# Performance work log

Hardware: AMD Instinct MI355X
Metric: run time of the kernel (lower is better)

Reference implementation:

```python
import jax, jax.numpy as jnp
import numpy as np

B, M, D, H, C = 256, 512, 768, 8, 768


def setup_inputs() -> dict:
    key = jax.random.key(0)
    ks = jax.random.split(key, 12)
    rn = lambda k, shp, s=1.0: jax.random.normal(k, shp, dtype=jnp.float32) * s
    w = 1.0 / np.sqrt(D)
    return dict(
        controller_state=rn(ks[0], (B, C)),
        write_data=rn(ks[1], (B, D)),
        memory=rn(ks[2], (M, D), 0.1),
        in_proj_w=rn(ks[3], (3 * D, D), w), in_proj_b=jnp.zeros((3 * D,), jnp.float32),
        out_w=rn(ks[4], (D, D), w), out_b=jnp.zeros((D,), jnp.float32),
        read_w=rn(ks[5], (D, C), w), read_b=jnp.zeros((D,), jnp.float32),
        write_w=rn(ks[6], (D, C), w), write_b=jnp.zeros((D,), jnp.float32),
        erase_w=rn(ks[7], (D, C), w), erase_b=jnp.zeros((D,), jnp.float32),
        ug_w=rn(ks[8], (1, C + D), w), ug_b=jnp.zeros((1,), jnp.float32),
        fg_w=rn(ks[9], (1, C + D), w), fg_b=jnp.zeros((1,), jnp.float32),
    )


def _mha(q, kv, in_proj_w, in_proj_b, out_w, out_b, num_heads):
    # q: [B,1,D] query, kv: [B,M,D] keys=values. Matches torch.nn.MultiheadAttention
    # (batch_first, eval mode -> no dropout, average_attn_weights=True).
    b, m, d = kv.shape
    dh = d // num_heads
    wq, wk, wv = jnp.split(in_proj_w, 3, axis=0)
    bq, bk, bv = jnp.split(in_proj_b, 3, axis=0)
    qh = (q @ wq.T + bq).reshape(b, 1, num_heads, dh).transpose(0, 2, 1, 3)   # [B,H,1,dh]
    kh = (kv @ wk.T + bk).reshape(b, m, num_heads, dh).transpose(0, 2, 1, 3)  # [B,H,M,dh]
    vh = (kv @ wv.T + bv).reshape(b, m, num_heads, dh).transpose(0, 2, 1, 3)
    scores = jnp.einsum('bhqd,bhkd->bhqk', qh, kh) / jnp.sqrt(jnp.float32(dh))
    attn = jax.nn.softmax(scores, axis=-1)                                    # [B,H,1,M]
    ctx = jnp.einsum('bhqk,bhkd->bhqd', attn, vh)
    ctx = ctx.transpose(0, 2, 1, 3).reshape(b, 1, d)
    out = ctx @ out_w.T + out_b
    return out, attn.mean(axis=1)  # out [B,1,D], weights averaged over heads [B,1,M]


def reference(controller_state, write_data, memory, in_proj_w, in_proj_b,
              out_w, out_b, read_w, read_b, write_w, write_b,
              erase_w, erase_b, ug_w, ug_b, fg_w, fg_b):
    b = controller_state.shape[0]
    memory_batch = jnp.broadcast_to(memory[None], (b,) + memory.shape)        # [B,M,D]

    read_key = (controller_state @ read_w.T + read_b)[:, None, :]             # [B,1,D]
    read_data, _ = _mha(read_key, memory_batch, in_proj_w, in_proj_b, out_w, out_b, H)
    read_data = read_data[:, 0, :]                                            # [B,D]

    write_key = (controller_state @ write_w.T + write_b)[:, None, :]
    erase_vec = jax.nn.sigmoid(controller_state @ erase_w.T + erase_b)[:, None, :]  # [B,1,D]
    _, write_weights = _mha(write_key, memory_batch, in_proj_w, in_proj_b, out_w, out_b, H)
    ww = write_weights[:, 0, :]                                               # [B,M]

    combined = jnp.concatenate([controller_state, read_data], axis=-1)        # [B,C+D]
    ug = jax.nn.sigmoid(combined @ ug_w.T + ug_b)                             # [B,1]
    fg = jax.nn.sigmoid(combined @ fg_w.T + fg_b)                             # [B,1]

    erase_term = ww[:, :, None] * erase_vec * fg[:, :, None]                  # [B,M,D]
    write_term = ww[:, :, None] * write_data[:, None, :] * ug[:, :, None]     # [B,M,D]
    updated_memory = memory_batch + (write_term - erase_term)
    return read_data, updated_memory
```

## Files before the change

kernel.cpp:

```cpp
#include <hip/hip_runtime.h>
#include <hip/hip_bf16.h>
#include <math.h>

#define B_ 256
#define M_ 512
#define D_ 768
#define H_ 8
#define DH_ 96
#define C_ 768

typedef float  f32x4_t __attribute__((ext_vector_type(4)));
typedef short  s16x8   __attribute__((ext_vector_type(8)));
typedef unsigned short u16;

__device__ __forceinline__ u16 cvt_bf16(float f) {
    __hip_bfloat16 h = __float2bfloat16(f);
    union { __hip_bfloat16 h; u16 u; } v; v.h = h;
    return v.u;
}
__device__ __forceinline__ float bf16_f32(u16 h) {
    union { unsigned int u; float f; } v; v.u = ((unsigned int)h) << 16;
    return v.f;
}

#define ACC_INIT {{0,0,0,0},{0,0,0,0},{0,0,0,0},{0,0,0,0}}
#define SCALE_ 0.10206207261596577f

template<int BK>
__device__ __forceinline__ void mm64b(
    const u16* __restrict__ A, int lda, const u16* __restrict__ B, int ldb,
    int ksteps, int bRowClamp, u16* lA, u16* lB, f32x4_t* acc, int nfrag)
{
    constexpr int NL = BK / 32;
    const int t = threadIdx.x;
    const int srow = t >> 2, kq = t & 3;
    const int l = t & 63, w = t >> 6;
    const int brow = srow < bRowClamp ? srow : bRowClamp;

    s16x8 va[NL], vb[NL];
    #pragma unroll
    for (int c = 0; c < NL; ++c) {
        const int ko = (kq * NL + c) * 8;
        va[c] = *reinterpret_cast<const s16x8*>(A + (size_t)srow * lda + ko);
        vb[c] = *reinterpret_cast<const s16x8*>(B + (size_t)brow * ldb + ko);
    }

    for (int ks = 0; ks < ksteps; ++ks) {
        __syncthreads();
        #pragma unroll
        for (int c = 0; c < NL; ++c) {
            const int kb = kq * NL + c;
            *reinterpret_cast<s16x8*>(lA + (kb * 64 + srow) * 8) = va[c];
            *reinterpret_cast<s16x8*>(lB + (kb * 64 + srow) * 8) = vb[c];
        }
        __syncthreads();
        if (ks + 1 < ksteps) {
            #pragma unroll
            for (int c = 0; c < NL; ++c) {
                const int ko = (ks + 1) * BK + (kq * NL + c) * 8;
                va[c] = *reinterpret_cast<const s16x8*>(A + (size_t)srow * lda + ko);
                vb[c] = *reinterpret_cast<const s16x8*>(B + (size_t)brow * ldb + ko);
            }
        }
        #pragma unroll
        for (int ksub = 0; ksub < NL; ++ksub) {
            const int kb = (l >> 4) + ksub * 4;
            s16x8 af = *reinterpret_cast<const s16x8*>(lA + (kb * 64 + w * 16 + (l & 15)) * 8);
            #pragma unroll
            for (int nb = 0; nb < 4; ++nb) {
                if (nb < nfrag) {
                    s16x8 bf = *reinterpret_cast<const s16x8*>(lB + (kb * 64 + nb * 16 + (l & 15)) * 8);
                    acc[nb] = __builtin_amdgcn_mfma_f32_16x16x32_bf16(af, bf, acc[nb], 0, 0, 0);
                }
            }
        }
    }
}

__device__ __forceinline__ void epilogue_f32(
    const f32x4_t* acc, float* out, int ldo, int m0, int n0,
    const float* bias, int act, int nfrag)
{
    const int t = threadIdx.x, l = t & 63, w = t >> 6;
    const int mbase = m0 + w * 16 + (l >> 4) * 4;
    #pragma unroll
    for (int nb = 0; nb < 4; ++nb) {
        if (nb >= nfrag) break;
        const int col = n0 + nb * 16 + (l & 15);
        const float bv = bias ? bias[col] : 0.0f;
        #pragma unroll
        for (int r = 0; r < 4; ++r) {
            float v = acc[nb][r] + bv;
            if (act) v = 1.0f / (1.0f + expf(-v));
            out[(size_t)(mbase + r) * ldo + col] = v;
        }
    }
}

__device__ __forceinline__ void epilogue_bf16(
    const f32x4_t* acc, u16* out, int ldo, int m0, int n0,
    const float* bias, int nfrag)
{
    const int t = threadIdx.x, l = t & 63, w = t >> 6;
    const int mbase = m0 + w * 16 + (l >> 4) * 4;
    #pragma unroll
    for (int nb = 0; nb < 4; ++nb) {
        if (nb >= nfrag) break;
        const int col = n0 + nb * 16 + (l & 15);
        const float bv = bias ? bias[col] : 0.0f;
        #pragma unroll
        for (int r = 0; r < 4; ++r)
            out[(size_t)(mbase + r) * ldo + col] = cvt_bf16(acc[nb][r] + bv);
    }
}

__global__ __launch_bounds__(256) void conv_kernel(
    const float* __restrict__ mem, const float* __restrict__ cs,
    const float* __restrict__ ipw, const float* __restrict__ rw,
    const float* __restrict__ www, const float* __restrict__ ew,
    const float* __restrict__ outw, const float* __restrict__ outb,
    const float* __restrict__ ugw, const float* __restrict__ ugb,
    const float* __restrict__ fgw, const float* __restrict__ fgb,
    u16* __restrict__ memb, u16* __restrict__ csb, u16* __restrict__ ipwb,
    u16* __restrict__ rwb, u16* __restrict__ wwwb, u16* __restrict__ ewb,
    u16* __restrict__ outwb, float* __restrict__ vg, float* __restrict__ gc)
{
    __shared__ float sred[256];
    const int bid = blockIdx.x, t = threadIdx.x;

    if (bid < 2304) {
        const float* src; u16* dst; int base;
        if      (bid < 192)  { src = mem;  dst = memb;  base = bid; }
        else if (bid < 288)  { src = cs;   dst = csb;   base = bid - 192; }
        else if (bid < 1152) { src = ipw;  dst = ipwb;  base = bid - 288; }
        else if (bid < 1440) { src = rw;   dst = rwb;   base = bid - 1152; }
        else if (bid < 1728) { src = www;  dst = wwwb;  base = bid - 1440; }
        else if (bid < 2016) { src = ew;   dst = ewb;   base = bid - 1728; }
        else                 { src = outw; dst = outwb; base = bid - 2016; }
        const size_t i = ((size_t)base * 256 + t) * 8;
        float4 x = *reinterpret_cast<const float4*>(src + i);
        float4 y = *reinterpret_cast<const float4*>(src + i + 4);
        s16x8 o;
        o[0]=cvt_bf16(x.x); o[1]=cvt_bf16(x.y); o[2]=cvt_bf16(x.z); o[3]=cvt_bf16(x.w);
        o[4]=cvt_bf16(y.x); o[5]=cvt_bf16(y.y); o[6]=cvt_bf16(y.z); o[7]=cvt_bf16(y.w);
        *reinterpret_cast<s16x8*>(dst + i) = o;
    } else {
        const int lid = bid - 2304;
        const int v = lid / 12, kt = lid % 12;
        const float* gw = v == 0 ? ugw : fgw;
        const int c = t & 63, g = t >> 6;
        const int col = kt * 64 + c;
        float acc = 0.f;
        #pragma unroll 4
        for (int i = 0; i < 192; ++i) {
            const int row = g * 192 + i;
            acc += outw[(size_t)row * 768 + col] * gw[768 + row];
        }
        sred[t] = acc;
        __syncthreads();
        if (g == 0)
            vg[v * 768 + col] = sred[c] + sred[64 + c] + sred[128 + c] + sred[192 + c];
        if (kt == 0) {
            __syncthreads();
            float cp = outb[t] * gw[768 + t] + outb[t + 256] * gw[768 + t + 256]
                     + outb[t + 512] * gw[768 + t + 512];
            sred[t] = cp; __syncthreads();
            #pragma unroll
            for (int off = 128; off > 0; off >>= 1) {
                if (t < off) sred[t] += sred[t + off];
                __syncthreads();
            }
            if (t == 0) gc[v] = sred[0] + (v == 0 ? ugb[0] : fgb[0]);
        }
    }
}

__global__ __launch_bounds__(256) void stage1_kernel(
    const u16* __restrict__ memb, const u16* __restrict__ csb,
    const u16* __restrict__ ipwb, const float* __restrict__ ipb,
    const u16* __restrict__ rwb, const float* __restrict__ rb,
    const u16* __restrict__ wwwb, const float* __restrict__ ww_b,
    const u16* __restrict__ ewb, const float* __restrict__ eb,
    u16* __restrict__ khb, u16* __restrict__ vhT,
    u16* __restrict__ rwkeysb, float* __restrict__ erase)
{
    __shared__ u16 lA[8192], lB[8192];
    f32x4_t acc[4] = ACC_INIT;
    const int bid = blockIdx.x;
    if (bid < 192) {
        const int mt = bid / 24, nt = bid % 24;
        mm64b<64>(memb + (size_t)mt * 64 * 768, 768,
                  ipwb + (size_t)768 * 768 + (size_t)nt * 64 * 768, 768,
                  12, 63, lA, lB, acc, 4);
        const int t = threadIdx.x, l = t & 63, w = t >> 6;
        const int mbase = mt * 64 + w * 16 + (l >> 4) * 4;
        if (nt < 12) {
            #pragma unroll
            for (int nb = 0; nb < 4; ++nb) {
                const int col = nt * 64 + nb * 16 + (l & 15);
                const float bv = ipb[768 + col];
                #pragma unroll
                for (int r = 0; r < 4; ++r)
                    khb[(size_t)(mbase + r) * 768 + col] = cvt_bf16(acc[nb][r] + bv);
            }
        } else {
            #pragma unroll
            for (int nb = 0; nb < 4; ++nb) {
                const int cg = (nt - 12) * 64 + nb * 16 + (l & 15);
                const int h = cg / 96, d = cg % 96;
                const float bv = ipb[1536 + cg];
                u16* dst = vhT + ((size_t)h * 96 + d) * 512;
                #pragma unroll
                for (int r = 0; r < 4; ++r)
                    dst[mbase + r] = cvt_bf16(acc[nb][r] + bv);
            }
        }
    } else if (bid < 240) {
        const int lid = bid - 192, mt = lid / 12, nt = lid % 12;
        mm64b<64>(csb + (size_t)mt * 64 * 768, 768, rwb + (size_t)nt * 64 * 768, 768,
                  12, 63, lA, lB, acc, 4);
        epilogue_bf16(acc, rwkeysb, 768, mt * 64, nt * 64, rb, 4);
    } else if (bid < 288) {
        const int lid = bid - 240, mt = lid / 12, nt = lid % 12;
        mm64b<64>(csb + (size_t)mt * 64 * 768, 768, wwwb + (size_t)nt * 64 * 768, 768,
                  12, 63, lA, lB, acc, 4);
        epilogue_bf16(acc, rwkeysb + (size_t)256 * 768, 768, mt * 64, nt * 64, ww_b, 4);
    } else {
        const int lid = bid - 288, mt = lid / 12, nt = lid % 12;
        mm64b<64>(csb + (size_t)mt * 64 * 768, 768, ewb + (size_t)nt * 64 * 768, 768,
                  12, 63, lA, lB, acc, 4);
        epilogue_f32(acc, erase, 768, mt * 64, nt * 64, eb, 1, 4);
    }
}

__global__ __launch_bounds__(256) void stage2_kernel(
    const u16* __restrict__ rwkeysb, const u16* __restrict__ ipwb,
    const float* __restrict__ ipb, u16* __restrict__ qrwb)
{
    __shared__ u16 lA[8192], lB[8192];
    f32x4_t acc[4] = ACC_INIT;
    const int mt = blockIdx.x / 12, nt = blockIdx.x % 12;
    mm64b<64>(rwkeysb + (size_t)mt * 64 * 768, 768, ipwb + (size_t)nt * 64 * 768, 768,
              12, 63, lA, lB, acc, 4);
    epilogue_bf16(acc, qrwb, 768, mt * 64, nt * 64, ipb, 4);
}

__global__ __launch_bounds__(256) void scores_kernel(
    const u16* __restrict__ qrwb, const u16* __restrict__ khb, u16* __restrict__ E)
{
    __shared__ u16 lA[2048], lB[2048];
    f32x4_t acc[4] = ACC_INIT;
    const int h = blockIdx.y;
    const int mt = blockIdx.x >> 3, nt = blockIdx.x & 7;
    mm64b<32>(qrwb + (size_t)mt * 64 * 768 + h * 96, 768,
              khb + (size_t)nt * 64 * 768 + h * 96, 768, 3, 63, lA, lB, acc, 4);
    const int t = threadIdx.x, l = t & 63, w = t >> 6;
    const int mbase = mt * 64 + w * 16 + (l >> 4) * 4;
    #pragma unroll
    for (int nb = 0; nb < 4; ++nb) {
        const int col = nt * 64 + nb * 16 + (l & 15);
        #pragma unroll
        for (int r = 0; r < 4; ++r) {
            const float e = expf(fminf(acc[nb][r] * SCALE_, 30.0f));
            E[((size_t)h * 512 + mbase + r) * 512 + col] = cvt_bf16(e);
        }
    }
}

__global__ __launch_bounds__(256) void pv_kernel(
    const u16* __restrict__ E, const u16* __restrict__ vhT, u16* __restrict__ ctxb)
{
    __shared__ u16 lA[8192], lB[8192];
    __shared__ float rinv[64];
    f32x4_t acc[4] = ACC_INIT;
    const int h = blockIdx.z, mt = blockIdx.x, nt = blockIdx.y;
    const int n0 = nt * 64;
    const int nfrag = nt == 0 ? 4 : 2;
    const int bclamp = nt == 0 ? 63 : 31;

    const u16* A  = E + ((size_t)h * 512 + mt * 64) * 512;
    const u16* Bv = vhT + ((size_t)h * 96 + n0) * 512;

    const int t = threadIdx.x;
    const int srow = t >> 2, kq = t & 3;
    const int l = t & 63, w = t >> 6;
    const int brow = srow < bclamp ? srow : bclamp;

    s16x8 va[2], vb[2];
    #pragma unroll
    for (int c = 0; c < 2; ++c) {
        const int ko = (kq * 2 + c) * 8;
        va[c] = *reinterpret_cast<const s16x8*>(A + (size_t)srow * 512 + ko);
        vb[c] = *reinterpret_cast<const s16x8*>(Bv + (size_t)brow * 512 + ko);
    }

    float rs = 0.f;
    for (int ks = 0; ks < 8; ++ks) {
        __syncthreads();
        #pragma unroll
        for (int c = 0; c < 2; ++c) {
            const int kb = kq * 2 + c;
            *reinterpret_cast<s16x8*>(lA + (kb * 64 + srow) * 8) = va[c];
            *reinterpret_cast<s16x8*>(lB + (kb * 64 + srow) * 8) = vb[c];
        }
        #pragma unroll
        for (int c = 0; c < 2; ++c)
            #pragma unroll
            for (int j = 0; j < 8; ++j)
                rs += bf16_f32((u16)va[c][j]);
        __syncthreads();
        if (ks + 1 < 8) {
            #pragma unroll
            for (int c = 0; c < 2; ++c) {
                const int ko = (ks + 1) * 64 + (kq * 2 + c) * 8;
                va[c] = *reinterpret_cast<const s16x8*>(A + (size_t)srow * 512 + ko);
                vb[c] = *reinterpret_cast<const s16x8*>(Bv + (size_t)brow * 512 + ko);
            }
        }
        #pragma unroll
        for (int ksub = 0; ksub < 2; ++ksub) {
            const int kb = (l >> 4) + ksub * 4;
            s16x8 af = *reinterpret_cast<const s16x8*>(lA + (kb * 64 + w * 16 + (l & 15)) * 8);
            #pragma unroll
            for (int nb = 0; nb < 4; ++nb) {
                if (nb < nfrag) {
                    s16x8 bf = *reinterpret_cast<const s16x8*>(lB + (kb * 64 + nb * 16 + (l & 15)) * 8);
                    acc[nb] = __builtin_amdgcn_mfma_f32_16x16x32_bf16(af, bf, acc[nb], 0, 0, 0);
                }
            }
        }
    }
    rs += __shfl_xor(rs, 1);
    rs += __shfl_xor(rs, 2);
    if (kq == 0) rinv[srow] = 1.0f / rs;
    __syncthreads();

    const int mbase = w * 16 + (l >> 4) * 4;
    #pragma unroll
    for (int nb = 0; nb < 4; ++nb) {
        if (nb >= nfrag) break;
        const int col = n0 + nb * 16 + (l & 15);
        #pragma unroll
        for (int r = 0; r < 4; ++r) {
            const float v = acc[nb][r] * rinv[mbase + r];
            ctxb[(size_t)(mt * 64 + mbase + r) * 768 + h * 96 + col] = cvt_bf16(v);
        }
    }
}

__global__ __launch_bounds__(256) void gatesww_kernel(
    const u16* __restrict__ ctxb,
    const float* __restrict__ cs, const float* __restrict__ wdta,
    const float* __restrict__ erase,
    const float* __restrict__ ugw, const float* __restrict__ fgw,
    const float* __restrict__ vg, const float* __restrict__ gc,
    const u16* __restrict__ E,
    float* __restrict__ delta, float* __restrict__ wwb)
{
    const int bid = blockIdx.x, t = threadIdx.x;
    if (bid < 256) {
        const int b = bid;
        __shared__ float red[8];
        float pu = 0.f, pf = 0.f;
        #pragma unroll
        for (int c = 0; c < 3; ++c) {
            const int i = t + c * 256;
            const float cv = cs[(size_t)b * 768 + i];
            const float xv = bf16_f32(ctxb[(size_t)b * 768 + i]);
            pu += cv * ugw[i] + xv * vg[i];
            pf += cv * fgw[i] + xv * vg[768 + i];
        }
        const int w = t >> 6, l = t & 63;
        #pragma unroll
        for (int off = 32; off > 0; off >>= 1) {
            pu += __shfl_xor(pu, off);
            pf += __shfl_xor(pf, off);
        }
        if (l == 0) { red[w] = pu; red[4 + w] = pf; }
        __syncthreads();
        const float ug = 1.0f / (1.0f + expf(-(red[0] + red[1] + red[2] + red[3] + gc[0])));
        const float fg = 1.0f / (1.0f + expf(-(red[4] + red[5] + red[6] + red[7] + gc[1])));
        #pragma unroll
        for (int c = 0; c < 3; ++c) {
            const int i = t + c * 256;
            delta[(size_t)b * 768 + i] = wdta[(size_t)b * 768 + i] * ug
                                       - erase[(size_t)b * 768 + i] * fg;
        }
    } else {
        const int b = bid - 256;
        __shared__ float linv8[8];
        const int w = t >> 6, l = t & 63;
        #pragma unroll
        for (int hh = 0; hh < 2; ++hh) {
            const int h = w * 2 + hh;
            const u16* row = E + ((size_t)h * 512 + 256 + b) * 512;
            float s = 0.f;
            #pragma unroll
            for (int c = 0; c < 8; ++c) s += bf16_f32(row[c * 64 + l]);
            #pragma unroll
            for (int off = 32; off > 0; off >>= 1) s += __shfl_xor(s, off);
            if (l == 0) linv8[h] = 1.0f / s;
        }
        __syncthreads();
        #pragma unroll
        for (int mm_ = 0; mm_ < 2; ++mm_) {
            const int m = t + mm_ * 256;
            float s = 0.f;
            #pragma unroll
            for (int h = 0; h < H_; ++h)
                s += bf16_f32(E[((size_t)h * 512 + 256 + b) * 512 + m]) * linv8[h];
            wwb[(size_t)b * 512 + m] = s * 0.125f;
        }
    }
}

__global__ __launch_bounds__(256) void final_kernel(
    const u16* __restrict__ ctxb, const u16* __restrict__ outwb,
    const float* __restrict__ outb, float* __restrict__ rd_out,
    const float* __restrict__ mem, const float* __restrict__ wwb,
    const float* __restrict__ delta, float* __restrict__ mem_out)
{
    __shared__ u16 lA[8192], lB[8192];
    const int bid = blockIdx.x, t = threadIdx.x;
    if (bid < 48) {
        f32x4_t acc[4] = ACC_INIT;
        const int mt = bid / 12, nt = bid % 12;
        mm64b<64>(ctxb + (size_t)mt * 64 * 768, 768, outwb + (size_t)nt * 64 * 768, 768,
                  12, 63, lA, lB, acc, 4);
        epilogue_f32(acc, rd_out, 768, mt * 64, nt * 64, outb, 0, 4);
    } else {
        const int u = bid - 48;
        const int b  = u >> 6;
        const int m0 = (u & 63) << 3;
        const f32x4_t* m4 = reinterpret_cast<const f32x4_t*>(mem);
        f32x4_t* o4 = reinterpret_cast<f32x4_t*>(mem_out + (size_t)b * 393216);
        const float* drow = delta + (size_t)b * 768;
        #pragma unroll
        for (int ph = 0; ph < 6; ++ph) {
            const int c = t + ph * 256;
            const int m = m0 + c / 192;
            const int d4 = c % 192;
            const float w = wwb[(size_t)b * 512 + m];
            const f32x4_t dd = *reinterpret_cast<const f32x4_t*>(drow + d4 * 4);
            f32x4_t mm = m4[(size_t)m * 192 + d4];
            f32x4_t r = mm + w * dd;
            __builtin_nontemporal_store(r, &o4[(size_t)m * 192 + d4]);
        }
    }
}

extern "C" void kernel_launch(void* const* d_in, const int* in_sizes, int n_in,
                              void* d_out, int out_size, void* d_ws, size_t ws_size,
                              hipStream_t stream)
{
    const float* cs   = (const float*)d_in[0];
    const float* wdta = (const float*)d_in[1];
    const float* mem  = (const float*)d_in[2];
    const float* ipw  = (const float*)d_in[3];
    const float* ipb  = (const float*)d_in[4];
    const float* outw = (const float*)d_in[5];
    const float* outb = (const float*)d_in[6];
    const float* rw   = (const float*)d_in[7];
    const float* rb   = (const float*)d_in[8];
    const float* ww_w = (const float*)d_in[9];
    const float* ww_b = (const float*)d_in[10];
    const float* ew   = (const float*)d_in[11];
    const float* eb   = (const float*)d_in[12];
    const float* ugw  = (const float*)d_in[13];
    const float* ugb  = (const float*)d_in[14];
    const float* fgw  = (const float*)d_in[15];
    const float* fgb  = (const float*)d_in[16];

    float* rd_out  = (float*)d_out;
    float* mem_out = (float*)d_out + B_ * D_;

    float* S0 = mem_out;
    u16*   memb    = (u16*)(S0 + 0);
    u16*   csb     = (u16*)(S0 + 196608);
    u16*   ipwb    = (u16*)(S0 + 294912);
    u16*   rwb     = (u16*)(S0 + 1179648);
    u16*   wwwb    = (u16*)(S0 + 1474560);
    u16*   ewb     = (u16*)(S0 + 1769472);
    u16*   khb     = (u16*)(S0 + 2064384);
    u16*   vhT     = (u16*)(S0 + 2260992);
    u16*   rwkeysb = (u16*)(S0 + 2457600);
    u16*   qrwb    = (u16*)(S0 + 2654208);

    float* ws    = (float*)d_ws;
    float* erase = ws;
    u16*   ctxb  = (u16*)(ws + 196608);
    u16*   E     = (u16*)(ws + 294912);
    float* vg    =        ws + 1343488;
    float* gc    =        ws + 1345024;
    float* delta =        ws + 1345040;
    float* wwb   =        ws + 1541648;
    u16*   outwb = (u16*)(ws + 1672720);

    conv_kernel<<<2328, 256, 0, stream>>>(mem, cs, ipw, rw, ww_w, ew, outw, outb,
                                          ugw, ugb, fgw, fgb,
                                          memb, csb, ipwb, rwb, wwwb, ewb, outwb,
                                          vg, gc);
    stage1_kernel<<<336, 256, 0, stream>>>(memb, csb, ipwb, ipb, rwb, rb, wwwb, ww_b,
                                           ewb, eb, khb, vhT, rwkeysb, erase);
    stage2_kernel<<<96, 256, 0, stream>>>(rwkeysb, ipwb, ipb, qrwb);
    scores_kernel<<<dim3(64, 8), 256, 0, stream>>>(qrwb, khb, E);
    pv_kernel<<<dim3(4, 2, 8), 256, 0, stream>>>(E, vhT, ctxb);
    gatesww_kernel<<<512, 256, 0, stream>>>(ctxb, cs, wdta, erase, ugw, fgw, vg, gc,
                                            E, delta, wwb);
    final_kernel<<<16432, 256, 0, stream>>>(ctxb, outwb, outb, rd_out,
                                            mem, wwb, delta, mem_out);
}
```

Measured before the change: 139.0 us.

## Merge write-weight reduction into PV kernel and fold gate delta into final update

The write-weight head-average, which depends only on the scores matrix, now runs as extra blocks inside the PV kernel instead of waiting for ctx in the gates kernel. The gates kernel now emits only the two scalar gates per batch row. The final memory-update kernel computes write*ug - erase*fg inline rather than reading a precomputed delta buffer. This regroups the kernel dependency chain so independent work shares a launch and drops a delta write and read, at the cost of reloading two vectors per element in the final kernel.

```diff
diff --git a/kernel.cpp b/kernel.cpp
--- a/kernel.cpp
+++ b/kernel.cpp
@@ -267,127 +267,90 @@
     }
 }
 
-__global__ __launch_bounds__(256) void pv_kernel(
-    const u16* __restrict__ E, const u16* __restrict__ vhT, u16* __restrict__ ctxb)
-{
-    __shared__ u16 lA[8192], lB[8192];
-    __shared__ float rinv[64];
-    f32x4_t acc[4] = ACC_INIT;
-    const int h = blockIdx.z, mt = blockIdx.x, nt = blockIdx.y;
-    const int n0 = nt * 64;
-    const int nfrag = nt == 0 ? 4 : 2;
-    const int bclamp = nt == 0 ? 63 : 31;
-
-    const u16* A  = E + ((size_t)h * 512 + mt * 64) * 512;
-    const u16* Bv = vhT + ((size_t)h * 96 + n0) * 512;
-
-    const int t = threadIdx.x;
-    const int srow = t >> 2, kq = t & 3;
-    const int l = t & 63, w = t >> 6;
-    const int brow = srow < bclamp ? srow : bclamp;
-
-    s16x8 va[2], vb[2];
-    #pragma unroll
-    for (int c = 0; c < 2; ++c) {
-        const int ko = (kq * 2 + c) * 8;
-        va[c] = *reinterpret_cast<const s16x8*>(A + (size_t)srow * 512 + ko);
-        vb[c] = *reinterpret_cast<const s16x8*>(Bv + (size_t)brow * 512 + ko);
-    }
-
-    float rs = 0.f;
-    for (int ks = 0; ks < 8; ++ks) {
+__global__ __launch_bounds__(256) void pvww_kernel(
+    const u16* __restrict__ E, const u16* __restrict__ vhT, u16* __restrict__ ctxb,
+    float* __restrict__ wwb)
+{
+    const int bid = blockIdx.x, t = threadIdx.x;
+    if (bid < 64) {
+        __shared__ u16 lA[8192], lB[8192];
+        __shared__ float rinv[64];
+        f32x4_t acc[4] = ACC_INIT;
+        const int h = bid >> 3;
+        const int mt = (bid >> 1) & 3, nt = bid & 1;
+        const int n0 = nt * 64;
+        const int nfrag = nt == 0 ? 4 : 2;
+        const int bclamp = nt == 0 ? 63 : 31;
+
+        const u16* A  = E + ((size_t)h * 512 + mt * 64) * 512;
+        const u16* Bv = vhT + ((size_t)h * 96 + n0) * 512;
+
+        const int srow = t >> 2, kq = t & 3;
+        const int l = t & 63, w = t >> 6;
+        const int brow = srow < bclamp ? srow : bclamp;
+
+        s16x8 va[2], vb[2];
+        #pragma unroll
+        for (int c = 0; c < 2; ++c) {
+            const int ko = (kq * 2 + c) * 8;
+            va[c] = *reinterpret_cast<const s16x8*>(A + (size_t)srow * 512 + ko);
+            vb[c] = *reinterpret_cast<const s16x8*>(Bv + (size_t)brow * 512 + ko);
+        }
+
+        float rs = 0.f;
+        for (int ks = 0; ks < 8; ++ks) {
+            __syncthreads();
+            #pragma unroll
+            for (int c = 0; c < 2; ++c) {
+                const int kb = kq * 2 + c;
+                *reinterpret_cast<s16x8*>(lA + (kb * 64 + srow) * 8) = va[c];
+                *reinterpret_cast<s16x8*>(lB + (kb * 64 + srow) * 8) = vb[c];
+            }
+            #pragma unroll
+            for (int c = 0; c < 2; ++c)
+                #pragma unroll
+                for (int j = 0; j < 8; ++j)
+                    rs += bf16_f32((u16)va[c][j]);
+            __syncthreads();
+            if (ks + 1 < 8) {
+                #pragma unroll
+                for (int c = 0; c < 2; ++c) {
+                    const int ko = (ks + 1) * 64 + (kq * 2 + c) * 8;
+                    va[c] = *reinterpret_cast<const s16x8*>(A + (size_t)srow * 512 + ko);
+                    vb[c] = *reinterpret_cast<const s16x8*>(Bv + (size_t)brow * 512 + ko);
+                }
+            }
+            #pragma unroll
+            for (int ksub = 0; ksub < 2; ++ksub) {
+                const int kb = (l >> 4) + ksub * 4;
+                s16x8 af = *reinterpret_cast<const s16x8*>(lA + (kb * 64 + w * 16 + (l & 15)) * 8);
+                #pragma unroll
+                for (int nb = 0; nb < 4; ++nb) {
+                    if (nb < nfrag) {
+                        s16x8 bf = *reinterpret_cast<const s16x8*>(lB + (kb * 64 + nb * 16 + (l & 15)) * 8);
+                        acc[nb] = __builtin_amdgcn_mfma_f32_16x16x32_bf16(af, bf, acc[nb], 0, 0, 0);
+                    }
+                }
+            }
+        }
+        rs += __shfl_xor(rs, 1);
+        rs += __shfl_xor(rs, 2);
+        if (kq == 0) rinv[srow] = 1.0f / rs;
         __syncthreads();
-        #pragma unroll
-        for (int c = 0; c < 2; ++c) {
-            const int kb = kq * 2 + c;
-            *reinterpret_cast<s16x8*>(lA + (kb * 64 + srow) * 8) = va[c];
-            *reinterpret_cast<s16x8*>(lB + (kb * 64 + srow) * 8) = vb[c];
-        }
-        #pragma unroll
-        for (int c = 0; c < 2; ++c)
-            #pragma unroll
-            for (int j = 0; j < 8; ++j)
-                rs += bf16_f32((u16)va[c][j]);
-        __syncthreads();
-        if (ks + 1 < 8) {
-            #pragma unroll
-            for (int c = 0; c < 2; ++c) {
-                const int ko = (ks + 1) * 64 + (kq * 2 + c) * 8;
-                va[c] = *reinterpret_cast<const s16x8*>(A + (size_t)srow * 512 + ko);
-                vb[c] = *reinterpret_cast<const s16x8*>(Bv + (size_t)brow * 512 + ko);
-            }
-        }
-        #pragma unroll
-        for (int ksub = 0; ksub < 2; ++ksub) {
-            const int kb = (l >> 4) + ksub * 4;
-            s16x8 af = *reinterpret_cast<const s16x8*>(lA + (kb * 64 + w * 16 + (l & 15)) * 8);
-            #pragma unroll
-            for (int nb = 0; nb < 4; ++nb) {
-                if (nb < nfrag) {
-                    s16x8 bf = *reinterpret_cast<const s16x8*>(lB + (kb * 64 + nb * 16 + (l & 15)) * 8);
-                    acc[nb] = __builtin_amdgcn_mfma_f32_16x16x32_bf16(af, bf, acc[nb], 0, 0, 0);
-                }
-            }
-        }
-    }
-    rs += __shfl_xor(rs, 1);
-    rs += __shfl_xor(rs, 2);
-    if (kq == 0) rinv[srow] = 1.0f / rs;
-    __syncthreads();
-
-    const int mbase = w * 16 + (l >> 4) * 4;
-    #pragma unroll
-    for (int nb = 0; nb < 4; ++nb) {
-        if (nb >= nfrag) break;
-        const int col = n0 + nb * 16 + (l & 15);
-        #pragma unroll
-        for (int r = 0; r < 4; ++r) {
-            const float v = acc[nb][r] * rinv[mbase + r];
-            ctxb[(size_t)(mt * 64 + mbase + r) * 768 + h * 96 + col] = cvt_bf16(v);
-        }
-    }
-}
-
-__global__ __launch_bounds__(256) void gatesww_kernel(
-    const u16* __restrict__ ctxb,
-    const float* __restrict__ cs, const float* __restrict__ wdta,
-    const float* __restrict__ erase,
-    const float* __restrict__ ugw, const float* __restrict__ fgw,
-    const float* __restrict__ vg, const float* __restrict__ gc,
-    const u16* __restrict__ E,
-    float* __restrict__ delta, float* __restrict__ wwb)
-{
-    const int bid = blockIdx.x, t = threadIdx.x;
-    if (bid < 256) {
-        const int b = bid;
-        __shared__ float red[8];
-        float pu = 0.f, pf = 0.f;
-        #pragma unroll
-        for (int c = 0; c < 3; ++c) {
-            const int i = t + c * 256;
-            const float cv = cs[(size_t)b * 768 + i];
-            const float xv = bf16_f32(ctxb[(size_t)b * 768 + i]);
-            pu += cv * ugw[i] + xv * vg[i];
-            pf += cv * fgw[i] + xv * vg[768 + i];
-        }
-        const int w = t >> 6, l = t & 63;
-        #pragma unroll
-        for (int off = 32; off > 0; off >>= 1) {
-            pu += __shfl_xor(pu, off);
-            pf += __shfl_xor(pf, off);
-        }
-        if (l == 0) { red[w] = pu; red[4 + w] = pf; }
-        __syncthreads();
-        const float ug = 1.0f / (1.0f + expf(-(red[0] + red[1] + red[2] + red[3] + gc[0])));
-        const float fg = 1.0f / (1.0f + expf(-(red[4] + red[5] + red[6] + red[7] + gc[1])));
-        #pragma unroll
-        for (int c = 0; c < 3; ++c) {
-            const int i = t + c * 256;
-            delta[(size_t)b * 768 + i] = wdta[(size_t)b * 768 + i] * ug
-                                       - erase[(size_t)b * 768 + i] * fg;
+
+        const int mbase = w * 16 + (l >> 4) * 4;
+        #pragma unroll
+        for (int nb = 0; nb < 4; ++nb) {
+            if (nb >= nfrag) break;
+            const int col = n0 + nb * 16 + (l & 15);
+            #pragma unroll
+            for (int r = 0; r < 4; ++r) {
+                const float v = acc[nb][r] * rinv[mbase + r];
+                ctxb[(size_t)(mt * 64 + mbase + r) * 768 + h * 96 + col] = cvt_bf16(v);
+            }
         }
     } else {
-        const int b = bid - 256;
+        const int b = bid - 64;
         __shared__ float linv8[8];
         const int w = t >> 6, l = t & 63;
         #pragma unroll
@@ -414,11 +377,44 @@
     }
 }
 
+__global__ __launch_bounds__(256) void gates_kernel(
+    const u16* __restrict__ ctxb,
+    const float* __restrict__ cs,
+    const float* __restrict__ ugw, const float* __restrict__ fgw,
+    const float* __restrict__ vg, const float* __restrict__ gc,
+    float* __restrict__ ugfg)
+{
+    const int b = blockIdx.x, t = threadIdx.x;
+    __shared__ float red[8];
+    float pu = 0.f, pf = 0.f;
+    #pragma unroll
+    for (int c = 0; c < 3; ++c) {
+        const int i = t + c * 256;
+        const float cv = cs[(size_t)b * 768 + i];
+        const float xv = bf16_f32(ctxb[(size_t)b * 768 + i]);
+        pu += cv * ugw[i] + xv * vg[i];
+        pf += cv * fgw[i] + xv * vg[768 + i];
+    }
+    const int w = t >> 6, l = t & 63;
+    #pragma unroll
+    for (int off = 32; off > 0; off >>= 1) {
+        pu += __shfl_xor(pu, off);
+        pf += __shfl_xor(pf, off);
+    }
+    if (l == 0) { red[w] = pu; red[4 + w] = pf; }
+    __syncthreads();
+    if (t == 0) {
+        ugfg[2 * b]     = 1.0f / (1.0f + expf(-(red[0] + red[1] + red[2] + red[3] + gc[0])));
+        ugfg[2 * b + 1] = 1.0f / (1.0f + expf(-(red[4] + red[5] + red[6] + red[7] + gc[1])));
+    }
+}
+
 __global__ __launch_bounds__(256) void final_kernel(
     const u16* __restrict__ ctxb, const u16* __restrict__ outwb,
     const float* __restrict__ outb, float* __restrict__ rd_out,
     const float* __restrict__ mem, const float* __restrict__ wwb,
-    const float* __restrict__ delta, float* __restrict__ mem_out)
+    const float* __restrict__ wdta, const float* __restrict__ erase,
+    const float* __restrict__ ugfg, float* __restrict__ mem_out)
 {
     __shared__ u16 lA[8192], lB[8192];
     const int bid = blockIdx.x, t = threadIdx.x;
@@ -432,16 +428,20 @@
         const int u = bid - 48;
         const int b  = u >> 6;
         const int m0 = (u & 63) << 3;
+        const float ug = ugfg[2 * b], fg = ugfg[2 * b + 1];
         const f32x4_t* m4 = reinterpret_cast<const f32x4_t*>(mem);
         f32x4_t* o4 = reinterpret_cast<f32x4_t*>(mem_out + (size_t)b * 393216);
-        const float* drow = delta + (size_t)b * 768;
+        const float* wrow = wdta  + (size_t)b * 768;
+        const float* erow = erase + (size_t)b * 768;
         #pragma unroll
         for (int ph = 0; ph < 6; ++ph) {
             const int c = t + ph * 256;
             const int m = m0 + c / 192;
             const int d4 = c % 192;
             const float w = wwb[(size_t)b * 512 + m];
-            const f32x4_t dd = *reinterpret_cast<const f32x4_t*>(drow + d4 * 4);
+            const f32x4_t wd = *reinterpret_cast<const f32x4_t*>(wrow + d4 * 4);
+            const f32x4_t er = *reinterpret_cast<const f32x4_t*>(erow + d4 * 4);
+            const f32x4_t dd = wd * ug - er * fg;
             f32x4_t mm = m4[(size_t)m * 192 + d4];
             f32x4_t r = mm + w * dd;
             __builtin_nontemporal_store(r, &o4[(size_t)m * 192 + d4]);
@@ -492,9 +492,9 @@
     u16*   E     = (u16*)(ws + 294912);
     float* vg    =        ws + 1343488;
     float* gc    =        ws + 1345024;
-    float* delta =        ws + 1345040;
-    float* wwb   =        ws + 1541648;
-    u16*   outwb = (u16*)(ws + 1672720);
+    float* ugfg  =        ws + 1345040;
+    float* wwb   =        ws + 1345552;
+    u16*   outwb = (u16*)(ws + 1476624);
 
     conv_kernel<<<2328, 256, 0, stream>>>(mem, cs, ipw, rw, ww_w, ew, outw, outb,
                                           ugw, ugb, fgw, fgb,
@@ -504,9 +504,8 @@
                                            ewb, eb, khb, vhT, rwkeysb, erase);
     stage2_kernel<<<96, 256, 0, stream>>>(rwkeysb, ipwb, ipb, qrwb);
     scores_kernel<<<dim3(64, 8), 256, 0, stream>>>(qrwb, khb, E);
-    pv_kernel<<<dim3(4, 2, 8), 256, 0, stream>>>(E, vhT, ctxb);
-    gatesww_kernel<<<512, 256, 0, stream>>>(ctxb, cs, wdta, erase, ugw, fgw, vg, gc,
-                                            E, delta, wwb);
+    pvww_kernel<<<320, 256, 0, stream>>>(E, vhT, ctxb, wwb);
+    gates_kernel<<<256, 256, 0, stream>>>(ctxb, cs, ugw, fgw, vg, gc, ugfg);
     final_kernel<<<16432, 256, 0, stream>>>(ctxb, outwb, outb, rd_out,
-                                            mem, wwb, delta, mem_out);
-}
+                                            mem, wwb, wdta, erase, ugfg, mem_out);
+}
```

Result: faster. 126.6 us (-8.9%).
